# Kernel optimization log

Measured on AMD Instinct MI355X. Metric: run time of the kernel, lower is better.

Reference implementation:

```python
import jax, jax.numpy as jnp
import numpy as np

N, N2, N3 = 40000, 20000, 10000
E, E2, E3 = 640000, 320000, 160000
HEADS = 4
F_IN = 5


def _glorot(k, shape):
    lim = float(np.sqrt(6.0 / (shape[0] + shape[-1])))
    return jax.random.uniform(k, shape, jnp.float32, -lim, lim)


def setup_inputs() -> dict:
    key = jax.random.key(0)
    ks = jax.random.split(key, 40)
    inp = {}
    inp["x"] = jax.random.normal(ks[0], (N, F_IN), jnp.float32)
    inp["edge_index"] = jax.random.randint(ks[1], (2, E), 0, N)
    inp["edge_index2"] = jax.random.randint(ks[2], (2, E2), 0, N2)
    inp["edge_index3"] = jax.random.randint(ks[3], (2, E3), 0, N3)
    # graclus-style cluster maps; constructed surjective so no cluster is empty
    inp["cluster1"] = jax.random.permutation(ks[4], jnp.arange(N) % N2)
    inp["cluster2"] = jax.random.permutation(ks[5], jnp.arange(N2) % N3)
    dims = [(F_IN, 16), (16, 32), (32, 64), (64, 32), (64, 16)]
    i = 6
    for idx, (fi, fo) in enumerate(dims, 1):
        inp[f"cW{idx}"] = _glorot(ks[i], (fi, HEADS * fo)); i += 1
        inp[f"cU{idx}"] = _glorot(ks[i], (fi, HEADS)); i += 1
        inp[f"cc{idx}"] = jnp.zeros((HEADS,), jnp.float32)
        inp[f"cb{idx}"] = jnp.zeros((fo,), jnp.float32)
    inp["l1W"] = _glorot(ks[i], (32, 256)); i += 1
    inp["l1b"] = jnp.zeros((256,), jnp.float32)
    inp["l2W"] = _glorot(ks[i], (256, 6890)); i += 1
    inp["l2b"] = jnp.zeros((6890,), jnp.float32)
    inp["oW"] = _glorot(ks[i], (6890, 1)); i += 1
    inp["ob"] = jnp.zeros((1,), jnp.float32)
    return inp


def feast_conv(x, ei, W, U, c, b, n, fo):
    """PyG FeaStConv: self-loops, per-edge head-softmax attention, mean aggregation."""
    sl = jnp.arange(n)
    src = jnp.concatenate([ei[0], sl])  # message sources (x_j)
    dst = jnp.concatenate([ei[1], sl])  # aggregation targets (x_i)
    xs, xd = x[src], x[dst]
    q = jax.nn.softmax((xs - xd) @ U + c, axis=-1)          # [E+n, H]
    m = (xs @ W).reshape(-1, HEADS, fo)                      # [E+n, H, fo]
    msg = jnp.einsum('eh,eho->eo', q, m)                     # [E+n, fo]
    agg = jax.ops.segment_sum(msg, dst, num_segments=n)
    cnt = jax.ops.segment_sum(jnp.ones((dst.shape[0],), x.dtype), dst, num_segments=n)
    return agg / cnt[:, None] + b


def _forward(x, edge_index, edge_index2, edge_index3, cluster1, cluster2, p):
    x1 = jax.nn.relu(feast_conv(x, edge_index, p["cW1"], p["cU1"], p["cc1"], p["cb1"], N, 16))
    x2 = jax.ops.segment_max(x1, cluster1, num_segments=N2)                     # graclus max_pool
    x2 = jax.nn.relu(feast_conv(x2, edge_index2, p["cW2"], p["cU2"], p["cc2"], p["cb2"], N2, 32))
    x3 = jax.ops.segment_max(x2, cluster2, num_segments=N3)
    x3 = jax.nn.relu(feast_conv(x3, edge_index3, p["cW3"], p["cU3"], p["cc3"], p["cb3"], N3, 64))
    x3 = jax.nn.relu(feast_conv(x3, edge_index3, p["cW4"], p["cU4"], p["cc4"], p["cb4"], N3, 32))
    x3 = jnp.concatenate([x2, x3[cluster2]], axis=1)                            # [N2, 64] unpool+skip
    x3 = jax.nn.relu(feast_conv(x3, edge_index2, p["cW5"], p["cU5"], p["cc5"], p["cb5"], N2, 16))
    h = jnp.concatenate([x1, x3[cluster1]], axis=1)                             # [N, 32]
    h = jax.nn.relu(h @ p["l1W"] + p["l1b"])
    h = jax.nn.relu(h @ p["l2W"] + p["l2b"])                                   # [N, 6890]
    return jax.nn.sigmoid(h @ p["oW"] + p["ob"])                                # [N, 1]


def reference(x, edge_index, edge_index2, edge_index3, cluster1, cluster2,
              cW1, cU1, cc1, cb1, cW2, cU2, cc2, cb2, cW3, cU3, cc3, cb3,
              cW4, cU4, cc4, cb4, cW5, cU5, cc5, cb5, l1W, l1b, l2W, l2b, oW, ob):
    p = dict(cW1=cW1, cU1=cU1, cc1=cc1, cb1=cb1, cW2=cW2, cU2=cU2, cc2=cc2, cb2=cb2,
             cW3=cW3, cU3=cU3, cc3=cc3, cb3=cb3, cW4=cW4, cU4=cU4, cc4=cc4, cb4=cb4,
             cW5=cW5, cU5=cU5, cc5=cc5, cb5=cb5, l1W=l1W, l1b=l1b, l2W=l2W, l2b=l2b,
             oW=oW, ob=ob)
    return _forward(x, edge_index, edge_index2, edge_index3, cluster1, cluster2, p)
```

## Files before the change

### kernel.cpp

```cpp
#include <hip/hip_runtime.h>
#include <math.h>

#define N1  40000
#define NN2 20000
#define NN3 10000
#define EE1 640000
#define EE2 320000
#define EE3 160000
#define ET  (EE1 + EE2 + EE3)
#define JPAD 6912
#define JREAL 6890
#define NTILE 432
#define CSPLIT 8
#define TPB (NTILE/CSPLIT)
#define NSTG (TPB/2)
#define NROWP 40192
#define NGRP 628
#define CAP 64

typedef __attribute__((ext_vector_type(8))) short short8;
typedef __attribute__((ext_vector_type(4))) float f32x4;

__device__ inline unsigned short f2bf(float f) {
  unsigned u = __float_as_uint(f);
  u += 0x7FFF + ((u >> 16) & 1);
  return (unsigned short)(u >> 16);
}

__device__ inline f32x4 qsoft(f32x4 xs, f32x4 xd, float c0, float c1, float c2, float c3) {
  float l0 = xs[0] - xd[0] + c0, l1 = xs[1] - xd[1] + c1;
  float l2 = xs[2] - xd[2] + c2, l3 = xs[3] - xd[3] + c3;
  float mx = fmaxf(fmaxf(l0, l1), fmaxf(l2, l3));
  float q0 = __expf(l0 - mx), q1 = __expf(l1 - mx);
  float q2 = __expf(l2 - mx), q3 = __expf(l3 - mx);
  float iv = 1.f / (q0 + q1 + q2 + q3);
  return (f32x4){q0 * iv, q1 * iv, q2 * iv, q3 * iv};
}

__global__ void k_matmulWU(const float* __restrict__ Xa, int fa,
                           const float* __restrict__ Xb, int fb,
                           const int* __restrict__ map,
                           const float* __restrict__ W, const float* __restrict__ U,
                           float* __restrict__ xW, float* __restrict__ xU,
                           int n, int co) {
  int ct = co + 4;
  int idx = blockIdx.x * 256 + threadIdx.x;
  if (idx >= n * ct) return;
  int row = idx / ct, col = idx - row * ct;
  const float* M;
  int stride;
  if (col < co) { M = W + col; stride = co; }
  else          { M = U + (col - co); stride = 4; }
  float s = 0.f;
  const float* ar = Xa + (size_t)row * fa;
  for (int k = 0; k < fa; ++k) s = fmaf(ar[k], M[(size_t)k * stride], s);
  if (Xb) {
    const float* br = Xb + (size_t)map[row] * fb;
    for (int k = 0; k < fb; ++k) s = fmaf(br[k], M[(size_t)(fa + k) * stride], s);
  }
  if (col < co) xW[(size_t)row * co + col] = s;
  else          xU[(size_t)row * 4 + (col - co)] = s;
}

__global__ void k_xU(const float* __restrict__ xin, const float* __restrict__ U,
                     float* __restrict__ xu, int n, int ci) {
  int idx = blockIdx.x * 256 + threadIdx.x;
  if (idx >= n * 4) return;
  int h = idx & 3, d = idx >> 2;
  const float* xr = xin + (size_t)d * ci;
  float s = 0.f;
  for (int k = 0; k < ci; ++k) s = fmaf(xr[k], U[k * 4 + h], s);
  xu[idx] = s;
}

__global__ void k_prep(const int* __restrict__ ei1, const int* __restrict__ ei2,
                       const int* __restrict__ ei3,
                       int* __restrict__ c1, int* __restrict__ c2, int* __restrict__ c3,
                       int* __restrict__ s1, int* __restrict__ s2, int* __restrict__ s3,
                       const float* __restrict__ x, float* __restrict__ x8,
                       const float* __restrict__ U1, float* __restrict__ xu1) {
  int i = blockIdx.x * 256 + threadIdx.x;
  if (i < ET) {
    int e = i;
    const int* ei; int* cnt; int* sl; int E;
    if (e < EE1) { ei = ei1; cnt = c1; sl = s1; E = EE1; }
    else {
      e -= EE1;
      if (e < EE2) { ei = ei2; cnt = c2; sl = s2; E = EE2; }
      else { e -= EE2; ei = ei3; cnt = c3; sl = s3; E = EE3; }
    }
    int s = ei[e], d = ei[E + e];
    int pos = atomicAdd(&cnt[d], 1);
    if (pos < CAP) sl[(size_t)d * CAP + pos] = s;
    return;
  }
  i -= ET;
  if (i < N1 * 8) {
    int d = i >> 3, k = i & 7;
    x8[i] = (k < 5) ? x[d * 5 + k] : 0.f;
    return;
  }
  i -= N1 * 8;
  if (i < N1 * 4) {
    int h = i & 3, d = i >> 2;
    const float* xr = x + (size_t)d * 5;
    float s = 0.f;
#pragma unroll
    for (int k = 0; k < 5; ++k) s = fmaf(xr[k], U1[k * 4 + h], s);
    xu1[i] = s;
  }
}

__global__ void k_aggX(const int* __restrict__ cnt, const int* __restrict__ slots,
                       const float* __restrict__ xU, const f32x4* __restrict__ xin4,
                       int stride4, const float* __restrict__ c,
                       f32x4* __restrict__ agg4, int n, int ci4) {
  int idx = blockIdx.x * 256 + threadIdx.x;
  if (idx >= n * ci4 * 4) return;
  const int sp = idx & 3;
  int t = idx >> 2;
  const int cg = t % ci4, d = t / ci4;
  const float c0 = c[0], c1 = c[1], c2 = c[2], c3 = c[3];
  const f32x4* XU4 = (const f32x4*)xU;
  const f32x4 xd = XU4[d];
  const int deg = min(cnt[d], CAP);
  const int jlo = (deg * sp) >> 2, jhi = (deg * (sp + 1)) >> 2;
  const int* sl = slots + (size_t)d * CAP;
  f32x4 acc[4];
#pragma unroll
  for (int e = 0; e < 4; ++e) acc[e] = (f32x4){0.f, 0.f, 0.f, 0.f};
  int j = jlo;
  for (; j + 4 <= jhi; j += 4) {
    int s0 = sl[j], s1 = sl[j + 1], s2 = sl[j + 2], s3 = sl[j + 3];
    f32x4 u0 = XU4[s0], u1 = XU4[s1], u2 = XU4[s2], u3 = XU4[s3];
    f32x4 v0 = xin4[(size_t)s0 * stride4 + cg];
    f32x4 v1 = xin4[(size_t)s1 * stride4 + cg];
    f32x4 v2 = xin4[(size_t)s2 * stride4 + cg];
    f32x4 v3 = xin4[(size_t)s3 * stride4 + cg];
    f32x4 q0 = qsoft(u0, xd, c0, c1, c2, c3);
    f32x4 q1 = qsoft(u1, xd, c0, c1, c2, c3);
    f32x4 q2 = qsoft(u2, xd, c0, c1, c2, c3);
    f32x4 q3 = qsoft(u3, xd, c0, c1, c2, c3);
#pragma unroll
    for (int e = 0; e < 4; ++e)
      acc[e] += v0[e] * q0 + v1[e] * q1 + v2[e] * q2 + v3[e] * q3;
  }
  for (; j < jhi; ++j) {
    int s = sl[j];
    f32x4 u = XU4[s];
    f32x4 v = xin4[(size_t)s * stride4 + cg];
    f32x4 q = qsoft(u, xd, c0, c1, c2, c3);
#pragma unroll
    for (int e = 0; e < 4; ++e) acc[e] += v[e] * q;
  }
#pragma unroll
  for (int e = 0; e < 4; ++e)
#pragma unroll
    for (int h = 0; h < 4; ++h) {
      acc[e][h] += __shfl_xor(acc[e][h], 1);
      acc[e][h] += __shfl_xor(acc[e][h], 2);
    }
  if (sp) return;
  {
    float mx = fmaxf(fmaxf(c0, c1), fmaxf(c2, c3));
    float q0 = __expf(c0 - mx), q1 = __expf(c1 - mx);
    float q2 = __expf(c2 - mx), q3 = __expf(c3 - mx);
    float iv = 1.f / (q0 + q1 + q2 + q3);
    f32x4 q = (f32x4){q0 * iv, q1 * iv, q2 * iv, q3 * iv};
    f32x4 xv = xin4[(size_t)d * stride4 + cg];
#pragma unroll
    for (int e = 0; e < 4; ++e) acc[e] += xv[e] * q;
  }
  f32x4* dst = agg4 + (size_t)d * (ci4 * 4) + cg * 4;
#pragma unroll
  for (int e = 0; e < 4; ++e) dst[e] = acc[e];
}

__global__ void k_postW(const f32x4* __restrict__ agg4, int aggstride, int kreal,
                        const float* __restrict__ W, const float* __restrict__ b,
                        const int* __restrict__ cnt, float* __restrict__ outp,
                        int n, int fo,
                        const int* __restrict__ pool_cl, int* __restrict__ pool_out) {
  int idx = blockIdx.x * 256 + threadIdx.x;
  if (idx >= n * fo) return;
  int o = idx % fo, d = idx / fo;
  const int co = 4 * fo;
  const f32x4* ar = agg4 + (size_t)d * aggstride;
  float acc = 0.f;
  for (int k = 0; k < kreal; ++k) {
    f32x4 f = ar[k];
    const float* wr = W + (size_t)k * co + o;
    acc += f[0] * wr[0] + f[1] * wr[fo] + f[2] * wr[2 * fo] + f[3] * wr[3 * fo];
  }
  int deg = min(cnt[d], CAP);
  float v = fmaxf(acc / (float)(deg + 1) + b[o], 0.f);
  outp[idx] = v;
  if (pool_cl)
    atomicMax((int*)&pool_out[(size_t)pool_cl[d] * fo + o], __float_as_int(v));
}

__global__ void k_attagg4(const int* __restrict__ cnt, const int* __restrict__ slots,
                          const float* __restrict__ xU, const float4* __restrict__ xW,
                          const float* __restrict__ c, const float4* __restrict__ b4,
                          float4* __restrict__ outp, int n, int fo4,
                          const int* __restrict__ pool_cl, int* __restrict__ pool_out) {
  int idx = blockIdx.x * 256 + threadIdx.x;
  if (idx >= n * fo4 * 4) return;
  const int sp = idx & 3;
  const int t = idx >> 2;
  const int d = t / fo4, og = t - d * fo4;
  const float c0 = c[0], c1 = c[1], c2 = c[2], c3 = c[3];
  const float4 xd = *(const float4*)&xU[(size_t)d * 4];
  const int deg = min(cnt[d], CAP);
  const int jlo = (deg * sp) >> 2;
  const int jhi = (deg * (sp + 1)) >> 2;
  const int* sl = slots + (size_t)d * CAP;
  float ax = 0.f, ay = 0.f, az = 0.f, aw = 0.f;
  int j = jlo;
  for (; j + 2 <= jhi; j += 2) {
    int sA = sl[j], sB = sl[j + 1];
    float4 xsA = *(const float4*)&xU[(size_t)sA * 4];
    float4 xsB = *(const float4*)&xU[(size_t)sB * 4];
    const float4* mA = xW + (size_t)sA * 4 * fo4 + og;
    const float4* mB = xW + (size_t)sB * 4 * fo4 + og;
    float4 a0 = mA[0], a1 = mA[fo4], a2 = mA[2 * fo4], a3 = mA[3 * fo4];
    float4 e0 = mB[0], e1 = mB[fo4], e2 = mB[2 * fo4], e3 = mB[3 * fo4];
    float lA0 = xsA.x - xd.x + c0, lA1 = xsA.y - xd.y + c1;
    float lA2 = xsA.z - xd.z + c2, lA3 = xsA.w - xd.w + c3;
    float mxA = fmaxf(fmaxf(lA0, lA1), fmaxf(lA2, lA3));
    float qA0 = __expf(lA0 - mxA), qA1 = __expf(lA1 - mxA);
    float qA2 = __expf(lA2 - mxA), qA3 = __expf(lA3 - mxA);
    float ivA = 1.f / (qA0 + qA1 + qA2 + qA3);
    qA0 *= ivA; qA1 *= ivA; qA2 *= ivA; qA3 *= ivA;
    float lB0 = xsB.x - xd.x + c0, lB1 = xsB.y - xd.y + c1;
    float lB2 = xsB.z - xd.z + c2, lB3 = xsB.w - xd.w + c3;
    float mxB = fmaxf(fmaxf(lB0, lB1), fmaxf(lB2, lB3));
    float qB0 = __expf(lB0 - mxB), qB1 = __expf(lB1 - mxB);
    float qB2 = __expf(lB2 - mxB), qB3 = __expf(lB3 - mxB);
    float ivB = 1.f / (qB0 + qB1 + qB2 + qB3);
    qB0 *= ivB; qB1 *= ivB; qB2 *= ivB; qB3 *= ivB;
    ax += qA0 * a0.x + qA1 * a1.x + qA2 * a2.x + qA3 * a3.x
        + qB0 * e0.x + qB1 * e1.x + qB2 * e2.x + qB3 * e3.x;
    ay += qA0 * a0.y + qA1 * a1.y + qA2 * a2.y + qA3 * a3.y
        + qB0 * e0.y + qB1 * e1.y + qB2 * e2.y + qB3 * e3.y;
    az += qA0 * a0.z + qA1 * a1.z + qA2 * a2.z + qA3 * a3.z
        + qB0 * e0.z + qB1 * e1.z + qB2 * e2.z + qB3 * e3.z;
    aw += qA0 * a0.w + qA1 * a1.w + qA2 * a2.w + qA3 * a3.w
        + qB0 * e0.w + qB1 * e1.w + qB2 * e2.w + qB3 * e3.w;
  }
  if (j < jhi) {
    int s = sl[j];
    float4 xs = *(const float4*)&xU[(size_t)s * 4];
    const float4* m = xW + (size_t)s * 4 * fo4 + og;
    float4 m0 = m[0], m1 = m[fo4], m2 = m[2 * fo4], m3 = m[3 * fo4];
    float l0 = xs.x - xd.x + c0, l1 = xs.y - xd.y + c1;
    float l2 = xs.z - xd.z + c2, l3 = xs.w - xd.w + c3;
    float mx = fmaxf(fmaxf(l0, l1), fmaxf(l2, l3));
    float q0 = __expf(l0 - mx), q1 = __expf(l1 - mx);
    float q2 = __expf(l2 - mx), q3 = __expf(l3 - mx);
    float inv = 1.f / (q0 + q1 + q2 + q3);
    q0 *= inv; q1 *= inv; q2 *= inv; q3 *= inv;
    ax += q0 * m0.x + q1 * m1.x + q2 * m2.x + q3 * m3.x;
    ay += q0 * m0.y + q1 * m1.y + q2 * m2.y + q3 * m3.y;
    az += q0 * m0.z + q1 * m1.z + q2 * m2.z + q3 * m3.z;
    aw += q0 * m0.w + q1 * m1.w + q2 * m2.w + q3 * m3.w;
  }
  ax += __shfl_xor(ax, 1); ay += __shfl_xor(ay, 1);
  az += __shfl_xor(az, 1); aw += __shfl_xor(aw, 1);
  ax += __shfl_xor(ax, 2); ay += __shfl_xor(ay, 2);
  az += __shfl_xor(az, 2); aw += __shfl_xor(aw, 2);
  if (sp) return;
  {
    float mx = fmaxf(fmaxf(c0, c1), fmaxf(c2, c3));
    float q0 = __expf(c0 - mx), q1 = __expf(c1 - mx);
    float q2 = __expf(c2 - mx), q3 = __expf(c3 - mx);
    float inv = 1.f / (q0 + q1 + q2 + q3);
    const float4* m = xW + (size_t)d * 4 * fo4 + og;
    float4 m0 = m[0], m1 = m[fo4], m2 = m[2 * fo4], m3 = m[3 * fo4];
    ax += (q0 * m0.x + q1 * m1.x + q2 * m2.x + q3 * m3.x) * inv;
    ay += (q0 * m0.y + q1 * m1.y + q2 * m2.y + q3 * m3.y) * inv;
    az += (q0 * m0.z + q1 * m1.z + q2 * m2.z + q3 * m3.z) * inv;
    aw += (q0 * m0.w + q1 * m1.w + q2 * m2.w + q3 * m3.w) * inv;
  }
  const float inv = 1.f / (float)(deg + 1);
  const float4 bb = b4[og];
  float4 v;
  v.x = fmaxf(ax * inv + bb.x, 0.f);
  v.y = fmaxf(ay * inv + bb.y, 0.f);
  v.z = fmaxf(az * inv + bb.z, 0.f);
  v.w = fmaxf(aw * inv + bb.w, 0.f);
  outp[(size_t)d * fo4 + og] = v;
  if (pool_cl) {
    int* po = pool_out + ((size_t)pool_cl[d] * fo4 + og) * 4;
    atomicMax(&po[0], __float_as_int(v.x));
    atomicMax(&po[1], __float_as_int(v.y));
    atomicMax(&po[2], __float_as_int(v.z));
    atomicMax(&po[3], __float_as_int(v.w));
  }
}

__global__ __launch_bounds__(256) void k_packB(
    const float* __restrict__ l2W, short8* __restrict__ Bp,
    const float* __restrict__ l2b, const float* __restrict__ oW,
    float* __restrict__ l2bp, float* __restrict__ oWp) {
  __shared__ float tile[32][65];
  const int bid = blockIdx.x, tid = threadIdx.x;
  if (bid < 27) {
    int j = bid * 256 + tid;
    l2bp[j] = (j < JREAL) ? l2b[j] : 0.f;
    oWp[j]  = (j < JREAL) ? oW[j]  : 0.f;
  }
  const int kg = bid / 108, jg = bid - kg * 108;
  const int k0 = kg * 32, j0 = jg * 64;
  const int kr = tid >> 6, jc = tid & 63;
  const int j = j0 + jc;
#pragma unroll
  for (int i = 0; i < 8; ++i) {
    int row = kr * 8 + i;
    tile[row][jc] = (j < JREAL) ? l2W[(size_t)(k0 + row) * JREAL + j] : 0.f;
  }
  __syncthreads();
  const int tt = tid >> 6, lane = tid & 63;
  short8 v;
#pragma unroll
  for (int i = 0; i < 8; ++i)
    v[i] = (short)f2bf(tile[((lane >> 4) << 3) + i][tt * 16 + (lane & 15)]);
  Bp[((size_t)(jg * 4 + tt) * 8 + kg) * 64 + lane] = v;
}

__global__ __launch_bounds__(256) void k_packh(
    const float* __restrict__ x1, const float* __restrict__ x5,
    const int* __restrict__ cl1, const float* __restrict__ l1W,
    const float* __restrict__ l1b, short8* __restrict__ Apack) {
  __shared__ float h1s[64][256];
  const int tid = threadIdx.x;
  const int row0 = blockIdx.x * 64;

  float wcol[32];
#pragma unroll
  for (int k = 0; k < 32; ++k) wcol[k] = l1W[k * 256 + tid];
  const float bt = l1b[tid];

  for (int r = 0; r < 64; ++r) {
    const int row = row0 + r;
    float s = bt;
    if (row < N1) {
      const float* a = x1 + (size_t)row * 16;
      const float* b = x5 + (size_t)cl1[row] * 16;
#pragma unroll
      for (int k = 0; k < 16; ++k) s = fmaf(a[k], wcol[k], s);
#pragma unroll
      for (int k = 0; k < 16; ++k) s = fmaf(b[k], wcol[16 + k], s);
    }
    h1s[r][tid ^ ((r & 7) << 3)] = fmaxf(s, 0.f);
  }
  __syncthreads();

#pragma unroll
  for (int j = 0; j < 8; ++j) {
    int s = j * 256 + tid;
    int l = s & 63, ks = (s >> 6) & 7, rb = s >> 9;
    int row = rb * 16 + (l & 15);
    int col0 = (ks * 32 + ((l >> 4) << 3)) ^ ((row & 7) << 3);
    const float* sp = &h1s[row][col0];
    short8 v;
#pragma unroll
    for (int i = 0; i < 8; ++i) v[i] = (short)f2bf(sp[i]);
    Apack[(size_t)blockIdx.x * 2048 + s] = v;
  }
}

__global__ __launch_bounds__(256, 2) void k_final2(
    const short8* __restrict__ Apack, const short8* __restrict__ Bp,
    const float* __restrict__ l2bp, const float* __restrict__ oWp,
    float* __restrict__ zbuf) {
  __shared__ short8 bufs[2][1024];
  const int tid = threadIdx.x, wid = tid >> 6, l = tid & 63;
  const int rg = blockIdx.x >> 3, cg = blockIdx.x & 7;
  const int lm = l & 15, lh = l >> 4;

  short8 af[4][8];
  {
    const short8* ap = Apack + (size_t)(rg * 4 + wid) * 2048 + l;
#pragma unroll
    for (int rb = 0; rb < 4; ++rb)
#pragma unroll
      for (int ks = 0; ks < 8; ++ks) af[rb][ks] = ap[rb * 512 + ks * 64];
  }

  const short8* bsrc = Bp + (size_t)cg * TPB * 512;
  short8 n0 = bsrc[tid], n1 = bsrc[256 + tid], n2 = bsrc[512 + tid], n3 = bsrc[768 + tid];
  bufs[0][tid] = n0; bufs[0][256 + tid] = n1;
  bufs[0][512 + tid] = n2; bufs[0][768 + tid] = n3;
  {
    const short8* p = bsrc + 1024;
    n0 = p[tid]; n1 = p[256 + tid]; n2 = p[512 + tid]; n3 = p[768 + tid];
  }
  asm volatile("s_waitcnt lgkmcnt(0)" ::: "memory");
  __builtin_amdgcn_s_barrier();
  asm volatile("" ::: "memory");

  float zp[4][4];
#pragma unroll
  for (int rb = 0; rb < 4; ++rb)
#pragma unroll
    for (int r = 0; r < 4; ++r) zp[rb][r] = 0.f;

  for (int st = 0; st < NSTG; ++st) {
    const int cur = st & 1;
    if (st + 1 < NSTG) {
      bufs[cur ^ 1][tid] = n0; bufs[cur ^ 1][256 + tid] = n1;
      bufs[cur ^ 1][512 + tid] = n2; bufs[cur ^ 1][768 + tid] = n3;
    }
    if (st + 2 < NSTG) {
      const short8* p = bsrc + (st + 2) * 1024;
      n0 = p[tid]; n1 = p[256 + tid]; n2 = p[512 + tid]; n3 = p[768 + tid];
    }
#pragma unroll
    for (int half = 0; half < 2; ++half) {
      short8 bfr[8];
#pragma unroll
      for (int ks = 0; ks < 8; ++ks) bfr[ks] = bufs[cur][half * 512 + ks * 64 + l];

      f32x4 acc[4];
#pragma unroll
      for (int rb = 0; rb < 4; ++rb) acc[rb] = (f32x4){0.f, 0.f, 0.f, 0.f};
      __builtin_amdgcn_s_setprio(1);
#pragma unroll
      for (int ks = 0; ks < 8; ++ks)
#pragma unroll
        for (int rb = 0; rb < 4; ++rb)
          acc[rb] = __builtin_amdgcn_mfma_f32_16x16x32_bf16(af[rb][ks], bfr[ks], acc[rb], 0, 0, 0);
      __builtin_amdgcn_s_setprio(0);

      const int j = (cg * TPB + st * 2 + half) * 16 + lm;
      const float lb = l2bp[j];
      const float ow = oWp[j];
#pragma unroll
      for (int rb = 0; rb < 4; ++rb)
#pragma unroll
        for (int r = 0; r < 4; ++r)
          zp[rb][r] += fmaxf(acc[rb][r] + lb, 0.f) * ow;
    }
    asm volatile("s_waitcnt lgkmcnt(0)" ::: "memory");
    __builtin_amdgcn_s_barrier();
    asm volatile("" ::: "memory");
  }

#pragma unroll
  for (int m = 1; m < 16; m <<= 1)
#pragma unroll
    for (int rb = 0; rb < 4; ++rb)
#pragma unroll
      for (int r = 0; r < 4; ++r)
        zp[rb][r] += __shfl_xor(zp[rb][r], m);

  if (lm == 0) {
    const int rbase = rg * 256 + wid * 64 + lh * 4;
#pragma unroll
    for (int rb = 0; rb < 4; ++rb)
#pragma unroll
      for (int r = 0; r < 4; ++r)
        atomicAdd(&zbuf[rbase + rb * 16 + r], zp[rb][r]);
  }
}

__global__ void k_sigm(const float* __restrict__ zbuf, const float* __restrict__ ob,
                       float* __restrict__ out) {
  int i = blockIdx.x * 256 + threadIdx.x;
  if (i >= N1) return;
  out[i] = 1.f / (1.f + expf(-(zbuf[i] + ob[0])));
}

static void run_conv(const float* xa, int fa, const float* xb, int fb, const int* gmap,
                     const int* cnt, const int* slots, int n, int fo,
                     const float* W, const float* U, const float* c, const float* b,
                     float* outp, float* xW, float* xU,
                     const int* pool_cl, int* pool_out, hipStream_t stream) {
  int co = 4 * fo;
  k_matmulWU<<<(n * (co + 4) + 255) / 256, 256, 0, stream>>>(xa, fa, xb, fb, gmap,
                                                             W, U, xW, xU, n, co);
  k_attagg4<<<(n * (fo / 4) * 4 + 255) / 256, 256, 0, stream>>>(
      cnt, slots, xU, (const float4*)xW, c, (const float4*)b, (float4*)outp, n, fo / 4,
      pool_cl, pool_out);
}

static void run_conv_agg(const float* xin_pad4, int stride4, int ci, int ci4,
                         const int* cnt, const int* slots, int n, int fo,
                         const float* W, const float* c, const float* b,
                         float* outp, const float* xu, float* aggbuf,
                         const int* pool_cl, int* pool_out, hipStream_t stream) {
  k_aggX<<<(n * ci4 * 4 + 255) / 256, 256, 0, stream>>>(
      cnt, slots, xu, (const f32x4*)xin_pad4, stride4, c, (f32x4*)aggbuf, n, ci4);
  k_postW<<<(n * fo + 255) / 256, 256, 0, stream>>>(
      (const f32x4*)aggbuf, ci4 * 4, ci, W, b, cnt, outp, n, fo, pool_cl, pool_out);
}

extern "C" void kernel_launch(void* const* d_in, const int* in_sizes, int n_in,
                              void* d_out, int out_size, void* d_ws, size_t ws_size,
                              hipStream_t stream) {
  const float* x   = (const float*)d_in[0];
  const int* ei1   = (const int*)d_in[1];
  const int* ei2   = (const int*)d_in[2];
  const int* ei3   = (const int*)d_in[3];
  const int* cl1   = (const int*)d_in[4];
  const int* cl2   = (const int*)d_in[5];
  const float* cW1 = (const float*)d_in[6],  *cU1 = (const float*)d_in[7],
             * cc1 = (const float*)d_in[8],  *cb1 = (const float*)d_in[9];
  const float* cW2 = (const float*)d_in[10], *cU2 = (const float*)d_in[11],
             * cc2 = (const float*)d_in[12], *cb2 = (const float*)d_in[13];
  const float* cW3 = (const float*)d_in[14], *cU3 = (const float*)d_in[15],
             * cc3 = (const float*)d_in[16], *cb3 = (const float*)d_in[17];
  const float* cW4 = (const float*)d_in[18], *cU4 = (const float*)d_in[19],
             * cc4 = (const float*)d_in[20], *cb4 = (const float*)d_in[21];
  const float* cW5 = (const float*)d_in[22], *cU5 = (const float*)d_in[23],
             * cc5 = (const float*)d_in[24], *cb5 = (const float*)d_in[25];
  const float* l1W = (const float*)d_in[26], *l1b = (const float*)d_in[27];
  const float* l2W = (const float*)d_in[28], *l2b = (const float*)d_in[29];
  const float* oW  = (const float*)d_in[30], *ob  = (const float*)d_in[31];

  float* ws = (float*)d_ws;
  float* x2p  = ws + 0;
  float* x3p  = ws + 320000;
  float* zbuf = ws + 640000;
  int*  cnt1  = (int*)(ws + 680192);
  int*  cnt2  = (int*)(ws + 720192);
  int*  cnt3  = (int*)(ws + 740192);
  int*  sl1   = (int*)(ws + 750192);
  int*  sl2   = (int*)(ws + 3310192);
  int*  sl3   = (int*)(ws + 4590192);
  float* x3a  = ws + 5230192;
  float* x3b  = ws + 5870192;
  float* x1   = ws + 6190192;
  float* x2   = ws + 6830192;
  float* x5   = ws + 7470192;
  short8* Bp  = (short8*)(ws + 7790192);
  float* l2bp = ws + 8674928;
  float* oWp  = ws + 8681840;
  float* xW   = ws + 8688752;
  float* xu   = ws + 11248752;
  float* x8   = ws + 11408752;
  float* aggbuf = ws + 11728752;
  short8* Apack = (short8*)(ws + 750192);

  hipMemsetAsync(ws, 0, 750192 * sizeof(float), stream);
  k_packB<<<864, 256, 0, stream>>>(l2W, Bp, l2b, oW, l2bp, oWp);

  k_prep<<<(ET + N1 * 8 + N1 * 4 + 255) / 256, 256, 0, stream>>>(
      ei1, ei2, ei3, cnt1, cnt2, cnt3, sl1, sl2, sl3, x, x8, cU1, xu);

  run_conv_agg(x8, 2, 5, 2, cnt1, sl1, N1, 16, cW1, cc1, cb1,
               x1, xu, aggbuf, cl1, (int*)x2p, stream);
  k_xU<<<(NN2 * 4 + 255) / 256, 256, 0, stream>>>(x2p, cU2, xu, NN2, 16);
  run_conv_agg(x2p, 4, 16, 4, cnt2, sl2, NN2, 32, cW2, cc2, cb2,
               x2, xu, aggbuf, cl2, (int*)x3p, stream);
  k_xU<<<(NN3 * 4 + 255) / 256, 256, 0, stream>>>(x3p, cU3, xu, NN3, 32);
  run_conv_agg(x3p, 8, 32, 8, cnt3, sl3, NN3, 64, cW3, cc3, cb3,
               x3a, xu, aggbuf, nullptr, nullptr, stream);
  run_conv(x3a, 64, nullptr, 0, nullptr, cnt3, sl3, NN3, 32,
           cW4, cU4, cc4, cb4, x3b, xW, xu, nullptr, nullptr, stream);
  run_conv(x2, 32, x3b, 32, cl2, cnt2, sl2, NN2, 16,
           cW5, cU5, cc5, cb5, x5, xW, xu, nullptr, nullptr, stream);

  k_packh<<<NGRP, 256, 0, stream>>>(x1, x5, cl1, l1W, l1b, Apack);
  k_final2<<<(NROWP / 256) * CSPLIT, 256, 0, stream>>>(Apack, Bp, l2bp, oWp, zbuf);
  k_sigm<<<(N1 + 255) / 256, 256, 0, stream>>>(zbuf, ob, (float*)d_out);
}
```

Before: 478.3 us.

## Fuse attention aggregation with post-weight matmul via shared memory per node block

Replaces the two-kernel path (aggregate inputs into a global buffer, then apply W) with one templated kernel. Each block aggregates several nodes into shared memory and then does the weight projection from there. This removes the intermediate global round-trip and one launch per conv. Conv4 is also switched from the transform-then-aggregate path to aggregate-then-transform, which needs a new xU kernel launch for it. The templated compile-time sizes allow loop unrolling, but the grid layouts change, and for conv4 the per-node matmul over 64 inputs may be heavy.

```diff
diff --git a/kernel.cpp b/kernel.cpp
--- a/kernel.cpp
+++ b/kernel.cpp
@@ -111,92 +111,102 @@
   }
 }
 
-__global__ void k_aggX(const int* __restrict__ cnt, const int* __restrict__ slots,
-                       const float* __restrict__ xU, const f32x4* __restrict__ xin4,
-                       int stride4, const float* __restrict__ c,
-                       f32x4* __restrict__ agg4, int n, int ci4) {
-  int idx = blockIdx.x * 256 + threadIdx.x;
-  if (idx >= n * ci4 * 4) return;
-  const int sp = idx & 3;
-  int t = idx >> 2;
-  const int cg = t % ci4, d = t / ci4;
+template<int CI4, int FO, int KREAL>
+__global__ __launch_bounds__(256) void k_aggf(
+    const int* __restrict__ cnt, const int* __restrict__ slots,
+    const float* __restrict__ xU, const f32x4* __restrict__ xin4, int stride4,
+    const float* __restrict__ c, const float* __restrict__ W,
+    const float* __restrict__ b, float* __restrict__ outp, int n,
+    const int* __restrict__ pool_cl, int* __restrict__ pool_out) {
+  constexpr int LPN = CI4 * 4;
+  constexpr int NB  = 256 / LPN;
+  __shared__ float sh[NB][CI4 * 16];
+  const int tid = threadIdx.x;
+  const int nl = tid / LPN, li = tid - nl * LPN;
+  const int cg = li >> 2, sp = li & 3;
+  const int d = blockIdx.x * NB + nl;
   const float c0 = c[0], c1 = c[1], c2 = c[2], c3 = c[3];
   const f32x4* XU4 = (const f32x4*)xU;
-  const f32x4 xd = XU4[d];
-  const int deg = min(cnt[d], CAP);
-  const int jlo = (deg * sp) >> 2, jhi = (deg * (sp + 1)) >> 2;
-  const int* sl = slots + (size_t)d * CAP;
-  f32x4 acc[4];
-#pragma unroll
-  for (int e = 0; e < 4; ++e) acc[e] = (f32x4){0.f, 0.f, 0.f, 0.f};
-  int j = jlo;
-  for (; j + 4 <= jhi; j += 4) {
-    int s0 = sl[j], s1 = sl[j + 1], s2 = sl[j + 2], s3 = sl[j + 3];
-    f32x4 u0 = XU4[s0], u1 = XU4[s1], u2 = XU4[s2], u3 = XU4[s3];
-    f32x4 v0 = xin4[(size_t)s0 * stride4 + cg];
-    f32x4 v1 = xin4[(size_t)s1 * stride4 + cg];
-    f32x4 v2 = xin4[(size_t)s2 * stride4 + cg];
-    f32x4 v3 = xin4[(size_t)s3 * stride4 + cg];
-    f32x4 q0 = qsoft(u0, xd, c0, c1, c2, c3);
-    f32x4 q1 = qsoft(u1, xd, c0, c1, c2, c3);
-    f32x4 q2 = qsoft(u2, xd, c0, c1, c2, c3);
-    f32x4 q3 = qsoft(u3, xd, c0, c1, c2, c3);
+
+  if (d < n) {
+    const f32x4 xd = XU4[d];
+    const int deg = min(cnt[d], CAP);
+    const int jlo = (deg * sp) >> 2, jhi = (deg * (sp + 1)) >> 2;
+    const int* sl = slots + (size_t)d * CAP;
+    f32x4 acc[4];
+#pragma unroll
+    for (int e = 0; e < 4; ++e) acc[e] = (f32x4){0.f, 0.f, 0.f, 0.f};
+    int j = jlo;
+    for (; j + 4 <= jhi; j += 4) {
+      int s0 = sl[j], s1 = sl[j + 1], s2 = sl[j + 2], s3 = sl[j + 3];
+      f32x4 u0 = XU4[s0], u1 = XU4[s1], u2 = XU4[s2], u3 = XU4[s3];
+      f32x4 v0 = xin4[(size_t)s0 * stride4 + cg];
+      f32x4 v1 = xin4[(size_t)s1 * stride4 + cg];
+      f32x4 v2 = xin4[(size_t)s2 * stride4 + cg];
+      f32x4 v3 = xin4[(size_t)s3 * stride4 + cg];
+      f32x4 q0 = qsoft(u0, xd, c0, c1, c2, c3);
+      f32x4 q1 = qsoft(u1, xd, c0, c1, c2, c3);
+      f32x4 q2 = qsoft(u2, xd, c0, c1, c2, c3);
+      f32x4 q3 = qsoft(u3, xd, c0, c1, c2, c3);
+#pragma unroll
+      for (int e = 0; e < 4; ++e)
+        acc[e] += v0[e] * q0 + v1[e] * q1 + v2[e] * q2 + v3[e] * q3;
+    }
+    for (; j < jhi; ++j) {
+      int s = sl[j];
+      f32x4 u = XU4[s];
+      f32x4 v = xin4[(size_t)s * stride4 + cg];
+      f32x4 q = qsoft(u, xd, c0, c1, c2, c3);
+#pragma unroll
+      for (int e = 0; e < 4; ++e) acc[e] += v[e] * q;
+    }
 #pragma unroll
     for (int e = 0; e < 4; ++e)
-      acc[e] += v0[e] * q0 + v1[e] * q1 + v2[e] * q2 + v3[e] * q3;
-  }
-  for (; j < jhi; ++j) {
-    int s = sl[j];
-    f32x4 u = XU4[s];
-    f32x4 v = xin4[(size_t)s * stride4 + cg];
-    f32x4 q = qsoft(u, xd, c0, c1, c2, c3);
-#pragma unroll
-    for (int e = 0; e < 4; ++e) acc[e] += v[e] * q;
-  }
-#pragma unroll
-  for (int e = 0; e < 4; ++e)
-#pragma unroll
-    for (int h = 0; h < 4; ++h) {
-      acc[e][h] += __shfl_xor(acc[e][h], 1);
-      acc[e][h] += __shfl_xor(acc[e][h], 2);
-    }
-  if (sp) return;
-  {
-    float mx = fmaxf(fmaxf(c0, c1), fmaxf(c2, c3));
-    float q0 = __expf(c0 - mx), q1 = __expf(c1 - mx);
-    float q2 = __expf(c2 - mx), q3 = __expf(c3 - mx);
-    float iv = 1.f / (q0 + q1 + q2 + q3);
-    f32x4 q = (f32x4){q0 * iv, q1 * iv, q2 * iv, q3 * iv};
-    f32x4 xv = xin4[(size_t)d * stride4 + cg];
-#pragma unroll
-    for (int e = 0; e < 4; ++e) acc[e] += xv[e] * q;
-  }
-  f32x4* dst = agg4 + (size_t)d * (ci4 * 4) + cg * 4;
-#pragma unroll
-  for (int e = 0; e < 4; ++e) dst[e] = acc[e];
-}
-
-__global__ void k_postW(const f32x4* __restrict__ agg4, int aggstride, int kreal,
-                        const float* __restrict__ W, const float* __restrict__ b,
-                        const int* __restrict__ cnt, float* __restrict__ outp,
-                        int n, int fo,
-                        const int* __restrict__ pool_cl, int* __restrict__ pool_out) {
-  int idx = blockIdx.x * 256 + threadIdx.x;
-  if (idx >= n * fo) return;
-  int o = idx % fo, d = idx / fo;
-  const int co = 4 * fo;
-  const f32x4* ar = agg4 + (size_t)d * aggstride;
-  float acc = 0.f;
-  for (int k = 0; k < kreal; ++k) {
-    f32x4 f = ar[k];
-    const float* wr = W + (size_t)k * co + o;
-    acc += f[0] * wr[0] + f[1] * wr[fo] + f[2] * wr[2 * fo] + f[3] * wr[3 * fo];
-  }
-  int deg = min(cnt[d], CAP);
-  float v = fmaxf(acc / (float)(deg + 1) + b[o], 0.f);
-  outp[idx] = v;
-  if (pool_cl)
-    atomicMax((int*)&pool_out[(size_t)pool_cl[d] * fo + o], __float_as_int(v));
+#pragma unroll
+      for (int h = 0; h < 4; ++h) {
+        acc[e][h] += __shfl_xor(acc[e][h], 1);
+        acc[e][h] += __shfl_xor(acc[e][h], 2);
+      }
+    if (sp == 0) {
+      float mx = fmaxf(fmaxf(c0, c1), fmaxf(c2, c3));
+      float q0 = __expf(c0 - mx), q1 = __expf(c1 - mx);
+      float q2 = __expf(c2 - mx), q3 = __expf(c3 - mx);
+      float iv = 1.f / (q0 + q1 + q2 + q3);
+      f32x4 q = (f32x4){q0 * iv, q1 * iv, q2 * iv, q3 * iv};
+      f32x4 xv = xin4[(size_t)d * stride4 + cg];
+#pragma unroll
+      for (int e = 0; e < 4; ++e) {
+        f32x4 a = acc[e] + xv[e] * q;
+#pragma unroll
+        for (int h = 0; h < 4; ++h) sh[nl][(cg * 4 + e) * 4 + h] = a[h];
+      }
+    }
+  }
+  __syncthreads();
+
+  constexpr int NBFO = NB * FO;
+#pragma unroll
+  for (int base = 0; base < NBFO; base += 256) {
+    int i2 = base + tid;
+    if (i2 < NBFO) {
+      int ln = i2 / FO, o = i2 - ln * FO;
+      int d2 = blockIdx.x * NB + ln;
+      if (d2 < n) {
+        float acc2 = 0.f;
+        const float* shl = sh[ln];
+        for (int k = 0; k < KREAL; ++k) {
+          const float* wr = W + (size_t)k * (4 * FO) + o;
+          acc2 += shl[k * 4 + 0] * wr[0] + shl[k * 4 + 1] * wr[FO]
+                + shl[k * 4 + 2] * wr[2 * FO] + shl[k * 4 + 3] * wr[3 * FO];
+        }
+        int deg2 = min(cnt[d2], CAP);
+        float v = fmaxf(acc2 / (float)(deg2 + 1) + b[o], 0.f);
+        outp[(size_t)d2 * FO + o] = v;
+        if (pool_cl)
+          atomicMax((int*)&pool_out[(size_t)pool_cl[d2] * FO + o], __float_as_int(v));
+      }
+    }
+  }
 }
 
 __global__ void k_attagg4(const int* __restrict__ cnt, const int* __restrict__ slots,
@@ -485,17 +495,6 @@
       pool_cl, pool_out);
 }
 
-static void run_conv_agg(const float* xin_pad4, int stride4, int ci, int ci4,
-                         const int* cnt, const int* slots, int n, int fo,
-                         const float* W, const float* c, const float* b,
-                         float* outp, const float* xu, float* aggbuf,
-                         const int* pool_cl, int* pool_out, hipStream_t stream) {
-  k_aggX<<<(n * ci4 * 4 + 255) / 256, 256, 0, stream>>>(
-      cnt, slots, xu, (const f32x4*)xin_pad4, stride4, c, (f32x4*)aggbuf, n, ci4);
-  k_postW<<<(n * fo + 255) / 256, 256, 0, stream>>>(
-      (const f32x4*)aggbuf, ci4 * 4, ci, W, b, cnt, outp, n, fo, pool_cl, pool_out);
-}
-
 extern "C" void kernel_launch(void* const* d_in, const int* in_sizes, int n_in,
                               void* d_out, int out_size, void* d_ws, size_t ws_size,
                               hipStream_t stream) {
@@ -540,7 +539,6 @@
   float* xW   = ws + 8688752;
   float* xu   = ws + 11248752;
   float* x8   = ws + 11408752;
-  float* aggbuf = ws + 11728752;
   short8* Apack = (short8*)(ws + 750192);
 
   hipMemsetAsync(ws, 0, 750192 * sizeof(float), stream);
@@ -549,16 +547,17 @@
   k_prep<<<(ET + N1 * 8 + N1 * 4 + 255) / 256, 256, 0, stream>>>(
       ei1, ei2, ei3, cnt1, cnt2, cnt3, sl1, sl2, sl3, x, x8, cU1, xu);
 
-  run_conv_agg(x8, 2, 5, 2, cnt1, sl1, N1, 16, cW1, cc1, cb1,
-               x1, xu, aggbuf, cl1, (int*)x2p, stream);
+  k_aggf<2, 16, 5><<<(N1 + 31) / 32, 256, 0, stream>>>(
+      cnt1, sl1, xu, (const f32x4*)x8, 2, cc1, cW1, cb1, x1, N1, cl1, (int*)x2p);
   k_xU<<<(NN2 * 4 + 255) / 256, 256, 0, stream>>>(x2p, cU2, xu, NN2, 16);
-  run_conv_agg(x2p, 4, 16, 4, cnt2, sl2, NN2, 32, cW2, cc2, cb2,
-               x2, xu, aggbuf, cl2, (int*)x3p, stream);
+  k_aggf<4, 32, 16><<<(NN2 + 15) / 16, 256, 0, stream>>>(
+      cnt2, sl2, xu, (const f32x4*)x2p, 4, cc2, cW2, cb2, x2, NN2, cl2, (int*)x3p);
   k_xU<<<(NN3 * 4 + 255) / 256, 256, 0, stream>>>(x3p, cU3, xu, NN3, 32);
-  run_conv_agg(x3p, 8, 32, 8, cnt3, sl3, NN3, 64, cW3, cc3, cb3,
-               x3a, xu, aggbuf, nullptr, nullptr, stream);
-  run_conv(x3a, 64, nullptr, 0, nullptr, cnt3, sl3, NN3, 32,
-           cW4, cU4, cc4, cb4, x3b, xW, xu, nullptr, nullptr, stream);
+  k_aggf<8, 64, 32><<<(NN3 + 7) / 8, 256, 0, stream>>>(
+      cnt3, sl3, xu, (const f32x4*)x3p, 8, cc3, cW3, cb3, x3a, NN3, nullptr, nullptr);
+  k_xU<<<(NN3 * 4 + 255) / 256, 256, 0, stream>>>(x3a, cU4, xu, NN3, 64);
+  k_aggf<16, 32, 64><<<(NN3 + 3) / 4, 256, 0, stream>>>(
+      cnt3, sl3, xu, (const f32x4*)x3a, 16, cc4, cW4, cb4, x3b, NN3, nullptr, nullptr);
   run_conv(x2, 32, x3b, 32, cl2, cnt2, sl2, NN2, 16,
            cW5, cU5, cc5, cb5, x5, xW, xu, nullptr, nullptr, stream);
 
```

Measured after the change: 426.3 us. -10.9%, faster.
